# Kernel tuning notes

Hardware: AMD Instinct MI355X
Metric: run time of the kernel (lower is better)

## Reference

```python
import jax, jax.numpy as jnp
import numpy as np

N, T, HW = 32, 46, 128
VOCAB_Q, NUM_ANS = 96, 32
WVEC, RNN_DIM = 32, 128
CNN_DIM, G_DIM, F_DIM = 24, 256, 256
G_IN = 2 * (CNN_DIM + 2) + RNN_DIM  # 180
BN_EPS = 1e-5


def setup_inputs() -> dict:
    key = jax.random.key(0)
    ks = jax.random.split(key, 16)
    s = 0.05
    rn = lambda k, shape: jax.random.normal(k, shape, dtype=jnp.float32) * s
    z = lambda shape: jnp.zeros(shape, jnp.float32)
    o = lambda shape: jnp.ones(shape, jnp.float32)
    inp = {}
    inp['questions'] = jax.random.randint(ks[0], (N, T), 1, VOCAB_Q)  # no NULL padding -> last step is the valid hidden state
    inp['images'] = jax.random.normal(ks[1], (N, 3, HW, HW), dtype=jnp.float32)
    inp['embed_W'] = rn(ks[2], (VOCAB_Q, WVEC))
    inp['lstm_Wih'] = rn(ks[3], (4 * RNN_DIM, WVEC))
    inp['lstm_Whh'] = rn(ks[4], (4 * RNN_DIM, RNN_DIM))
    inp['lstm_bih'] = z((4 * RNN_DIM,))
    inp['lstm_bhh'] = z((4 * RNN_DIM,))
    inp['conv0_W'] = rn(ks[5], (CNN_DIM, 3, 3, 3))
    inp['conv0_b'] = z((CNN_DIM,))
    inp['bn0_g'] = o((CNN_DIM,))
    inp['bn0_b'] = z((CNN_DIM,))
    inp['convs_W'] = rn(ks[6], (3, CNN_DIM, CNN_DIM, 3, 3))
    inp['convs_b'] = z((3, CNN_DIM))
    inp['bns_g'] = o((3, CNN_DIM))
    inp['bns_b'] = z((3, CNN_DIM))
    inp['g0_W'] = rn(ks[7], (G_DIM, G_IN))
    inp['g0_b'] = z((G_DIM,))
    inp['gs_W'] = rn(ks[8], (3, G_DIM, G_DIM))
    inp['gs_b'] = z((3, G_DIM))
    inp['f0_W'] = rn(ks[9], (F_DIM, G_DIM))
    inp['f0_b'] = z((F_DIM,))
    inp['f1_W'] = rn(ks[10], (F_DIM, F_DIM))
    inp['f1_b'] = z((F_DIM,))
    inp['f2_W'] = rn(ks[11], (NUM_ANS, F_DIM))
    inp['f2_b'] = z((NUM_ANS,))
    return inp


def _dense(x, W, b):
    return x @ W.T + b


def _lstm_last(emb, Wih, Whh, bih, bhh):
    # emb: (N, T, D); single-layer LSTM, PyTorch gate order (i, f, g, o); return last hidden state
    n, h = emb.shape[0], Whh.shape[1]
    bias = bih + bhh

    def step(carry, x_t):
        hp, cp = carry
        zg = x_t @ Wih.T + hp @ Whh.T + bias
        i, f, g, o_ = jnp.split(zg, 4, axis=-1)
        c = jax.nn.sigmoid(f) * cp + jax.nn.sigmoid(i) * jnp.tanh(g)
        hn = jax.nn.sigmoid(o_) * jnp.tanh(c)
        return (hn, c), None

    init = (jnp.zeros((n, h), emb.dtype), jnp.zeros((n, h), emb.dtype))
    (h_last, _), _ = jax.lax.scan(step, init, jnp.swapaxes(emb, 0, 1))
    return h_last


def _conv_bn_relu(x, W, b, gamma, beta):
    # Conv2d(k=3, s=2, p=1) + BatchNorm2d (training-mode batch stats) + ReLU
    x = jax.lax.conv_general_dilated(x, W, window_strides=(2, 2), padding=((1, 1), (1, 1)),
                                     dimension_numbers=('NCHW', 'OIHW', 'NCHW'))
    x = x + b[None, :, None, None]
    mu = x.mean((0, 2, 3), keepdims=True)
    var = ((x - mu) ** 2).mean((0, 2, 3), keepdims=True)  # biased var, as torch BN
    x = (x - mu) * jax.lax.rsqrt(var + BN_EPS)
    x = x * gamma[None, :, None, None] + beta[None, :, None, None]
    return jax.nn.relu(x)


def _forward(questions, images, embed_W, lstm_Wih, lstm_Whh, lstm_bih, lstm_bhh,
             conv0_W, conv0_b, bn0_g, bn0_b, convs_W, convs_b, bns_g, bns_b,
             g0_W, g0_b, gs_W, gs_b, f0_W, f0_b, f1_W, f1_b, f2_W, f2_b):
    # question encoder
    q_feats = _lstm_last(embed_W[questions], lstm_Wih, lstm_Whh, lstm_bih, lstm_bhh)  # (N, rnn_dim)
    # CNN stem
    x = _conv_bn_relu(images, conv0_W, conv0_b, bn0_g, bn0_b)
    for i in range(3):
        x = _conv_bn_relu(x, convs_W[i], convs_b[i], bns_g[i], bns_b[i])
    n, c, h, w = x.shape
    m = h * w
    # append normalized coordinates
    xc = jnp.broadcast_to(jnp.linspace(0.0, 1.0, w, dtype=x.dtype).reshape(1, 1, 1, w), (n, 1, h, w))
    yc = jnp.broadcast_to(jnp.linspace(0.0, 1.0, h, dtype=x.dtype).reshape(1, 1, h, 1), (n, 1, h, w))
    objects = jnp.concatenate([x, xc, yc], axis=1).reshape(n, c + 2, m)
    objects = jnp.swapaxes(objects, 1, 2)  # (N, M, C+2)
    # all M^2 ordered pairs: pairs[n, i*M+j] = [obj_i, obj_j]
    feats1 = jnp.repeat(objects, m, axis=1)        # (N, M^2, C+2)
    feats2 = jnp.tile(objects, (1, m, 1))          # (N, M^2, C+2)
    q_rep = jnp.broadcast_to(q_feats[:, None, :], (n, m * m, q_feats.shape[-1]))
    g_in = jnp.concatenate([feats1, feats2, q_rep], axis=-1)  # (N, M^2, 180)
    # shared MLP g
    hidden = jax.nn.relu(_dense(g_in, g0_W, g0_b))
    for i in range(3):
        hidden = jax.nn.relu(_dense(hidden, gs_W[i], gs_b[i]))
    f_in = hidden.sum(axis=1)  # old-torch sum(1) kept dim then [:,0] -> (N, g_dim)
    # MLP f (dropout = identity at eval)
    hidden = jax.nn.relu(_dense(f_in, f0_W, f0_b))
    hidden = jax.nn.relu(_dense(hidden, f1_W, f1_b))
    return _dense(hidden, f2_W, f2_b)  # (N, num_answers)


def reference(questions, images, embed_W, lstm_Wih, lstm_Whh, lstm_bih, lstm_bhh,
              conv0_W, conv0_b, bn0_g, bn0_b, convs_W, convs_b, bns_g, bns_b,
              g0_W, g0_b, gs_W, gs_b, f0_W, f0_b, f1_W, f1_b, f2_W, f2_b):
    return _forward(questions, images, embed_W, lstm_Wih, lstm_Whh, lstm_bih, lstm_bhh,
                    conv0_W, conv0_b, bn0_g, bn0_b, convs_W, convs_b, bns_g, bns_b,
                    g0_W, g0_b, gs_W, gs_b, f0_W, f0_b, f1_W, f1_b, f2_W, f2_b)
```

## Files before the change

### kernel.cpp

```cpp
#include <hip/hip_runtime.h>

#define NB   32
#define TT   46
#define RNN  128
#define CDIM 24
#define GD   256
#define GIN  180

typedef __attribute__((ext_vector_type(8))) short  bf16x8;
typedef __attribute__((ext_vector_type(4))) short  s16x4;
typedef __attribute__((ext_vector_type(8))) unsigned short u16x8;
typedef __attribute__((ext_vector_type(4))) float  f32x4;

__device__ __forceinline__ unsigned short f2bf(float v) {
    unsigned u = __float_as_uint(v);
    u = u + 0x7fffu + ((u >> 16) & 1u);
    return (unsigned short)(u >> 16);
}

__device__ __forceinline__ void lstm_body(
    const int* __restrict__ q, const float* __restrict__ embW,
    const float* __restrict__ Wih, const float* __restrict__ Whh,
    const float* __restrict__ bih, const float* __restrict__ bhh,
    float* __restrict__ qf, int n)
{
    const int tid = threadIdx.x;
    __shared__ __align__(16) float xs[32], hs[RNN];
    __shared__ float zg[512];
    f32x4 wih[8], whh[32];
    {
        const f32x4* wp = (const f32x4*)(Wih + tid * 32);
#pragma unroll
        for (int j = 0; j < 8; j++) wih[j] = wp[j];
        const f32x4* hp = (const f32x4*)(Whh + tid * RNN);
#pragma unroll
        for (int j = 0; j < 32; j++) whh[j] = hp[j];
    }
    const float bias = bih[tid] + bhh[tid];
    float creg = 0.f;
    if (tid < RNN) hs[tid] = 0.f;
    float xr = (tid < 32) ? embW[q[n * TT] * 32 + tid] : 0.f;
    __syncthreads();
    for (int t = 0; t < TT; t++) {
        if (tid < 32) xs[tid] = xr;
        __syncthreads();
        if (tid < 32 && t + 1 < TT) xr = embW[q[n * TT + t + 1] * 32 + tid];
        const f32x4* h4 = (const f32x4*)hs;
        const f32x4* x4 = (const f32x4*)xs;
        f32x4 a0 = {0.f, 0.f, 0.f, 0.f}, a1 = a0, a2 = a0, a3 = a0;
#pragma unroll
        for (int j = 0; j < 8; j += 4) {
            a0 += wih[j] * x4[j];     a1 += wih[j + 1] * x4[j + 1];
            a2 += wih[j + 2] * x4[j + 2]; a3 += wih[j + 3] * x4[j + 3];
        }
#pragma unroll
        for (int j = 0; j < 32; j += 4) {
            a0 += whh[j] * h4[j];     a1 += whh[j + 1] * h4[j + 1];
            a2 += whh[j + 2] * h4[j + 2]; a3 += whh[j + 3] * h4[j + 3];
        }
        f32x4 a = (a0 + a1) + (a2 + a3);
        zg[tid] = bias + ((a[0] + a[1]) + (a[2] + a[3]));
        __syncthreads();
        if (tid < RNN) {
            float ig = 1.f / (1.f + __expf(-zg[tid]));
            float fg = 1.f / (1.f + __expf(-zg[RNN + tid]));
            float gg = tanhf(zg[2 * RNN + tid]);
            float og = 1.f / (1.f + __expf(-zg[3 * RNN + tid]));
            float cn = fg * creg + ig * gg;
            creg = cn;
            hs[tid] = og * tanhf(cn);
        }
        __syncthreads();
    }
    if (tid < RNN) qf[n * RNN + tid] = hs[tid];
}

template<int CIN, int TILE, bool BNIN, int BS>
__device__ __forceinline__ void conv_body(
    const float* __restrict__ in, const float* __restrict__ Wg,
    const float* __restrict__ bias,
    const float* __restrict__ pstats, const float* __restrict__ pg,
    const float* __restrict__ pb, float pinvM,
    float* __restrict__ out, float* __restrict__ stats,
    int HIN, int WIN, int HO, int WO, int tilesX, int bx)
{
    constexpr int NPIX = TILE * TILE;
    constexpr int CPG  = BS / NPIX;
    constexpr int COPT = 24 / CPG;
    constexpr int WPB  = BS / 64;
    constexpr int WPC  = NPIX / 64;
    constexpr int S  = 2 * TILE + 1;
    constexpr int SP = S + 1;
    __shared__ float in_t[CIN][S][SP];
    __shared__ float r1s[WPB][COPT], r2s[WPB][COPT];
    __shared__ float sc[CIN], sh[CIN];
    const int tid = threadIdx.x;
    const int tx = bx % tilesX;
    const int ty = (bx / tilesX) % tilesX;
    const int n  = bx / (tilesX * tilesX);

    if (BNIN) {
        if (tid < CIN) {
            float mu  = pstats[2 * tid] * pinvM;
            float var = pstats[2 * tid + 1] * pinvM - mu * mu;
            float rs  = rsqrtf(var + 1e-5f);
            sc[tid] = rs * pg[tid];
            sh[tid] = pb[tid] - mu * rs * pg[tid];
        }
        __syncthreads();
    }
    const int iy0 = ty * 2 * TILE - 1, ix0 = tx * 2 * TILE - 1;
    for (int idx = tid; idx < CIN * S * S; idx += BS) {
        int ci = idx / (S * S), r = idx % (S * S);
        int ry = r / S, rx = r % S;
        int gy = iy0 + ry, gx = ix0 + rx;
        float v = 0.f;
        if ((unsigned)gy < (unsigned)HIN && (unsigned)gx < (unsigned)WIN) {
            v = in[((size_t)(n * CIN + ci) * HIN + gy) * WIN + gx];
            if (BNIN) v = fmaxf(v * sc[ci] + sh[ci], 0.f);
        }
        in_t[ci][ry][rx] = v;
    }
    __syncthreads();

    const int p   = tid % NPIX;
    const int co0 = __builtin_amdgcn_readfirstlane((tid / NPIX) * COPT);
    const int ly  = (p / TILE) * 2, lx = (p % TILE) * 2;
    float acc[COPT];
#pragma unroll
    for (int c = 0; c < COPT; c++) acc[c] = bias[co0 + c];
    for (int ci = 0; ci < CIN; ci++) {
#pragma unroll
        for (int ky = 0; ky < 3; ky++) {
            const float* row = &in_t[ci][ly + ky][lx];
#pragma unroll
            for (int kx = 0; kx < 3; kx++) {
                float v = row[kx];
#pragma unroll
                for (int c = 0; c < COPT; c++)
                    acc[c] += v * Wg[(((co0 + c) * CIN + ci) * 3 + ky) * 3 + kx];
            }
        }
    }
    const int oy = ty * TILE + p / TILE, ox = tx * TILE + p % TILE;
#pragma unroll
    for (int c = 0; c < COPT; c++)
        out[((size_t)(n * 24 + co0 + c) * HO + oy) * WO + ox] = acc[c];

    const int lane = tid & 63, wv = tid >> 6;
#pragma unroll
    for (int c = 0; c < COPT; c++) {
        float s1 = acc[c], s2 = acc[c] * acc[c];
#pragma unroll
        for (int off = 1; off < 64; off <<= 1) {
            s1 += __shfl_xor(s1, off, 64);
            s2 += __shfl_xor(s2, off, 64);
        }
        if (lane == 0) { r1s[wv][c] = s1; r2s[wv][c] = s2; }
    }
    __syncthreads();
    if (tid < 24) {
        int cg = tid / COPT, slot = tid % COPT;
        float t1 = 0.f, t2 = 0.f;
#pragma unroll
        for (int u = 0; u < WPC; u++) { t1 += r1s[cg * WPC + u][slot]; t2 += r2s[cg * WPC + u][slot]; }
        atomicAdd(&stats[tid * 2],     t1);
        atomicAdd(&stats[tid * 2 + 1], t2);
    }
}

template<int CIN, int TILE, bool BNIN>
__global__ __launch_bounds__(256) void conv_tiled(
    const float* __restrict__ in, const float* __restrict__ Wg,
    const float* __restrict__ bias,
    const float* __restrict__ pstats, const float* __restrict__ pg,
    const float* __restrict__ pb, float pinvM,
    float* __restrict__ out, float* __restrict__ stats,
    int HIN, int WIN, int HO, int WO, int tilesX)
{
    conv_body<CIN, TILE, BNIN, 256>(in, Wg, bias, pstats, pg, pb, pinvM,
                                    out, stats, HIN, WIN, HO, WO, tilesX, blockIdx.x);
}

__global__ __launch_bounds__(512, 2) void fused_front(
    const int* __restrict__ q, const float* __restrict__ embW,
    const float* __restrict__ Wih, const float* __restrict__ Whh,
    const float* __restrict__ bih, const float* __restrict__ bhh,
    float* __restrict__ qf,
    const float* __restrict__ images, const float* __restrict__ c0W,
    const float* __restrict__ c0b, float* __restrict__ conv0o,
    float* __restrict__ stats,
    const float* __restrict__ gsW, unsigned short* __restrict__ Wbf)
{
    const int bx = blockIdx.x;
    if (bx < 32) {
        lstm_body(q, embW, Wih, Whh, bih, bhh, qf, bx);
    } else if (bx < 544) {
        conv_body<3, 16, false, 512>(images, c0W, c0b, nullptr, nullptr, nullptr, 0.f,
                                     conv0o, stats, 128, 128, 64, 64, 4, bx - 32);
    } else {
        int i = ((bx - 544) << 9) + threadIdx.x;
#pragma unroll
        for (int u = 0; u < 4; u++) {
            Wbf[i] = f2bf(gsW[i]);
            i += 96 * 512;
        }
    }
}

__global__ __launch_bounds__(256) void abqt_kernel(
    const float* __restrict__ feat,
    const float* __restrict__ stats, const float* __restrict__ g,
    const float* __restrict__ b, float invM,
    const float* __restrict__ qf,
    const float* __restrict__ g0W,
    const float* __restrict__ g0b,
    float* __restrict__ A, float* __restrict__ Bm, float* __restrict__ QT)
{
    const int n = blockIdx.x >> 2, iq = blockIdx.x & 3, k = threadIdx.x;
    __shared__ float wAB[256][53];
    __shared__ float wq[64][128];
    __shared__ float obj[16][28];
    __shared__ float qs[RNN];
    __shared__ float sc[24], sh[24];
    if (k < 24) {
        float mu  = stats[2 * k] * invM;
        float var = stats[2 * k + 1] * invM - mu * mu;
        float rs  = rsqrtf(var + 1e-5f);
        sc[k] = rs * g[k];
        sh[k] = b[k] - mu * rs * g[k];
    }
    if (k >= 128) qs[k - 128] = qf[n * RNN + (k - 128)];
    for (int idx = k; idx < 256 * 52; idx += 256) {
        int kr = idx / 52, c = idx % 52;
        wAB[kr][c] = g0W[kr * GIN + c];
    }
    for (int idx = k; idx < 64 * 128; idx += 256) {
        int r = idx >> 7, d = idx & 127;
        wq[r][d] = g0W[(((iq << 6) + r)) * GIN + 52 + d];
    }
    __syncthreads();
    for (int idx = k; idx < 24 * 16; idx += 256) {
        int c = idx >> 4, il = idx & 15;
        int i = (iq << 4) + il;
        float v = feat[(n * CDIM + c) * 64 + i];
        obj[il][c] = fmaxf(v * sc[c] + sh[c], 0.f);
    }
    if (k < 16) {
        int i = (iq << 4) + k;
        obj[k][24] = (float)(i & 7)  * (1.f / 7.f);
        obj[k][25] = (float)(i >> 3) * (1.f / 7.f);
        obj[k][26] = 0.f; obj[k][27] = 0.f;
    }
    __syncthreads();
    if (k < 64) {
        int kr = (iq << 6) + k;
        float qv = g0b[kr];
#pragma unroll
        for (int d = 0; d < RNN; d++) qv += wq[k][d] * qs[d];
        QT[(n << 8) + kr] = qv;
    }
    float wA[26], wB[26];
#pragma unroll
    for (int c = 0; c < 26; c++) { wA[c] = wAB[k][c]; wB[c] = wAB[k][26 + c]; }
    for (int il = 0; il < 16; il++) {
        const f32x4* op = (const f32x4*)obj[il];
        f32x4 r0 = op[0], r1 = op[1], r2 = op[2], r3 = op[3],
              r4 = op[4], r5 = op[5], r6 = op[6];
        float a = 0.f, bb = 0.f;
#pragma unroll
        for (int p = 0; p < 4; p++) {
            a += wA[p] * r0[p] + wA[4 + p] * r1[p] + wA[8 + p] * r2[p]
               + wA[12 + p] * r3[p] + wA[16 + p] * r4[p] + wA[20 + p] * r5[p];
            bb += wB[p] * r0[p] + wB[4 + p] * r1[p] + wB[8 + p] * r2[p]
                + wB[12 + p] * r3[p] + wB[16 + p] * r4[p] + wB[20 + p] * r5[p];
        }
        a += wA[24] * r6[0] + wA[25] * r6[1];
        bb += wB[24] * r6[0] + wB[25] * r6[1];
        int i = (iq << 4) + il;
        A [(((n << 6) + i) << 8) + k] = a;
        Bm[(((n << 6) + i) << 8) + k] = bb;
    }
}

__global__ __launch_bounds__(256, 2) void gs_fused(
    const float* __restrict__ A, const float* __restrict__ Bm, const float* __restrict__ QT,
    const unsigned short* __restrict__ Wb,
    const float* __restrict__ gsb,
    float* __restrict__ partial)
{
    __shared__ __align__(16) unsigned short Xs[128 * 256];
    __shared__ float AQ[2][256];
    __shared__ float biasv[3][256];
    const int raw = blockIdx.x;
    const int bb = (raw & 7) * 128 + (raw >> 3);
    const int n = bb >> 5, ip = bb & 31, tid = threadIdx.x;
    const int lane = tid & 63, w = tid >> 6, l15 = lane & 15, lh = lane >> 4;

    {
        float qt = QT[(n << 8) + tid];
        AQ[0][tid] = A[(((n << 6) + ip * 2)     << 8) + tid] + qt;
        AQ[1][tid] = A[(((n << 6) + ip * 2 + 1) << 8) + tid] + qt;
        biasv[0][tid] = gsb[tid];
        biasv[1][tid] = gsb[256 + tid];
        biasv[2][tid] = gsb[512 + tid];
    }
    __syncthreads();

#pragma unroll
    for (int it = 0; it < 16; it++) {
        int task = tid + (it << 8);
        int r = task >> 5, g = task & 31;
        int isub = r >> 6, j = r & 63;
        const f32x4* bp = (const f32x4*)(Bm + (((n << 6) + j) << 8) + (g << 3));
        f32x4 b0 = bp[0], b1 = bp[1];
        u16x8 pk;
        int c0 = g << 3;
#pragma unroll
        for (int p = 0; p < 4; p++) {
            pk[p]     = f2bf(fmaxf(b0[p] + AQ[isub][c0 + p], 0.f));
            pk[p + 4] = f2bf(fmaxf(b1[p] + AQ[isub][c0 + 4 + p], 0.f));
        }
        *(u16x8*)((char*)Xs + r * 512 + ((g ^ (r & 7)) << 4)) = pk;
    }

    f32x4 acc[4][8];
    const f32x4 zero4 = {0.f, 0.f, 0.f, 0.f};
    bf16x8 wa[4], wn[4], xa[8], xn[8];
    for (int layer = 0; layer < 3; layer++) {
#pragma unroll
        for (int tc = 0; tc < 4; tc++)
#pragma unroll
            for (int sl = 0; sl < 8; sl++) acc[tc][sl] = zero4;
        const unsigned short* wbase = Wb + (layer << 16)
                                    + (((w << 6) + l15) << 8) + (lh << 3);
#pragma unroll
        for (int tc = 0; tc < 4; tc++) wa[tc] = *(const bf16x8*)(wbase + (tc << 12));
        __syncthreads();
#pragma unroll
        for (int sl = 0; sl < 8; sl++) {
            int ar = (sl << 4) + l15;
            int au = lh ^ (ar & 7);
            xa[sl] = *(const bf16x8*)((const char*)Xs + ar * 512 + (au << 4));
        }
#pragma unroll
        for (int kb = 0; kb < 8; kb++) {
            if (kb < 7) {
#pragma unroll
                for (int tc = 0; tc < 4; tc++)
                    wn[tc] = *(const bf16x8*)(wbase + (tc << 12) + ((kb + 1) << 5));
#pragma unroll
                for (int sl = 0; sl < 8; sl++) {
                    int ar = (sl << 4) + l15;
                    int au = (((kb + 1) << 2) + lh) ^ (ar & 7);
                    xn[sl] = *(const bf16x8*)((const char*)Xs + ar * 512 + (au << 4));
                }
            }
#pragma unroll
            for (int tc = 0; tc < 4; tc++)
#pragma unroll
                for (int sl = 0; sl < 8; sl++)
                    acc[tc][sl] = __builtin_amdgcn_mfma_f32_16x16x32_bf16(
                        wa[tc], xa[sl], acc[tc][sl], 0, 0, 0);
            if (kb < 7) {
#pragma unroll
                for (int tc = 0; tc < 4; tc++) wa[tc] = wn[tc];
#pragma unroll
                for (int sl = 0; sl < 8; sl++) xa[sl] = xn[sl];
            }
        }
        if (layer < 2) {
            __syncthreads();
#pragma unroll
            for (int tc = 0; tc < 4; tc++) {
                int c0 = (w << 6) + (tc << 4) + (lh << 2);
                float b0 = biasv[layer][c0],     b1 = biasv[layer][c0 + 1];
                float b2 = biasv[layer][c0 + 2], b3 = biasv[layer][c0 + 3];
#pragma unroll
                for (int sl = 0; sl < 8; sl++) {
                    int row = (sl << 4) + l15;
                    s16x4 pk;
                    pk[0] = (short)f2bf(fmaxf(acc[tc][sl][0] + b0, 0.f));
                    pk[1] = (short)f2bf(fmaxf(acc[tc][sl][1] + b1, 0.f));
                    pk[2] = (short)f2bf(fmaxf(acc[tc][sl][2] + b2, 0.f));
                    pk[3] = (short)f2bf(fmaxf(acc[tc][sl][3] + b3, 0.f));
                    *(s16x4*)((char*)Xs + row * 512 + (((c0 >> 3) ^ (row & 7)) << 4)
                              + ((c0 & 7) << 1)) = pk;
                }
            }
        } else {
#pragma unroll
            for (int tc = 0; tc < 4; tc++) {
                int c0 = (w << 6) + (tc << 4) + (lh << 2);
                f32x4 cs;
#pragma unroll
                for (int p = 0; p < 4; p++) {
                    float bv = biasv[2][c0 + p];
                    float s = 0.f;
#pragma unroll
                    for (int sl = 0; sl < 8; sl++) s += fmaxf(acc[tc][sl][p] + bv, 0.f);
                    s += __shfl_xor(s, 1, 64);
                    s += __shfl_xor(s, 2, 64);
                    s += __shfl_xor(s, 4, 64);
                    s += __shfl_xor(s, 8, 64);
                    cs[p] = s;
                }
                if (l15 == 0) *(f32x4*)(partial + (size_t)bb * 256 + c0) = cs;
            }
        }
    }
}

__device__ __forceinline__ float dot256(const float* __restrict__ wr,
                                        const float* __restrict__ x)
{
    const f32x4* w4 = (const f32x4*)wr;
    const f32x4* x4 = (const f32x4*)x;
    f32x4 a0 = {0.f, 0.f, 0.f, 0.f}, a1 = a0, a2 = a0, a3 = a0;
#pragma unroll 8
    for (int c = 0; c < 64; c += 4) {
        f32x4 w0 = w4[c], w1 = w4[c + 1], w2 = w4[c + 2], w3 = w4[c + 3];
        f32x4 x0 = x4[c], x1 = x4[c + 1], x2 = x4[c + 2], x3 = x4[c + 3];
        a0 += w0 * x0; a1 += w1 * x1; a2 += w2 * x2; a3 += w3 * x3;
    }
    f32x4 a = (a0 + a1) + (a2 + a3);
    return (a[0] + a[1]) + (a[2] + a[3]);
}

__global__ __launch_bounds__(256) void f_mlp(
    const float* __restrict__ partial,
    const float* __restrict__ f0W, const float* __restrict__ f0b,
    const float* __restrict__ f1W, const float* __restrict__ f1b,
    const float* __restrict__ f2W, const float* __restrict__ f2b,
    float* __restrict__ out)
{
    const int n = blockIdx.x, k = threadIdx.x;
    __shared__ float fin[256], h1[256], h2[256];
    const float* pb = partial + (size_t)(n * 32) * 256 + k;
    float s0 = 0.f, s1 = 0.f, s2 = 0.f, s3 = 0.f;
#pragma unroll
    for (int b = 0; b < 32; b += 4) {
        s0 += pb[(b + 0) << 8];
        s1 += pb[(b + 1) << 8];
        s2 += pb[(b + 2) << 8];
        s3 += pb[(b + 3) << 8];
    }
    fin[k] = (s0 + s1) + (s2 + s3);
    __syncthreads();
    h1[k] = fmaxf(dot256(f0W + (k << 8), fin) + f0b[k], 0.f);
    __syncthreads();
    h2[k] = fmaxf(dot256(f1W + (k << 8), h1) + f1b[k], 0.f);
    __syncthreads();
    if (k < 32)
        out[(n << 5) + k] = dot256(f2W + (k << 8), h2) + f2b[k];
}

extern "C" void kernel_launch(void* const* d_in, const int* in_sizes, int n_in,
                              void* d_out, int out_size, void* d_ws, size_t ws_size,
                              hipStream_t stream)
{
    const int*   questions = (const int*)  d_in[0];
    const float* images = (const float*)d_in[1];
    const float* embW   = (const float*)d_in[2];
    const float* Wih    = (const float*)d_in[3];
    const float* Whh    = (const float*)d_in[4];
    const float* bih    = (const float*)d_in[5];
    const float* bhh    = (const float*)d_in[6];
    const float* c0W    = (const float*)d_in[7];
    const float* c0b    = (const float*)d_in[8];
    const float* bn0g   = (const float*)d_in[9];
    const float* bn0b   = (const float*)d_in[10];
    const float* csW    = (const float*)d_in[11];
    const float* csb    = (const float*)d_in[12];
    const float* bnsg   = (const float*)d_in[13];
    const float* bnsb   = (const float*)d_in[14];
    const float* g0W    = (const float*)d_in[15];
    const float* g0b    = (const float*)d_in[16];
    const float* gsW    = (const float*)d_in[17];
    const float* gsb    = (const float*)d_in[18];
    const float* f0W    = (const float*)d_in[19];
    const float* f0b    = (const float*)d_in[20];
    const float* f1W    = (const float*)d_in[21];
    const float* f1b    = (const float*)d_in[22];
    const float* f2W    = (const float*)d_in[23];
    const float* f2b    = (const float*)d_in[24];

    float* ws  = (float*)d_ws;
    float* out = (float*)d_out;

    float* conv0o = ws;
    float* conv1o = ws + 3145728;
    float* conv2o = ws + 3932160;
    float* conv3o = ws + 4128768;
    float* stats  = ws + 4177920;
    float* qf     = ws + 4178112;
    unsigned short* Wbf = (unsigned short*)(ws + 4182208);
    float* Abuf   = ws;
    float* Bbuf   = ws + 524288;
    float* QTb    = ws + 1048576;
    float* part   = ws + 1155072;

    hipMemsetAsync(stats, 0, 192 * sizeof(float), stream);

    fused_front<<<640, 512, 0, stream>>>(questions, embW, Wih, Whh, bih, bhh, qf,
                                         images, c0W, c0b, conv0o, stats, gsW, Wbf);
    conv_tiled<24, 8, true><<<512, 256, 0, stream>>>(
        conv0o, csW, csb, stats, bn0g, bn0b, 1.f / 131072.f,
        conv1o, stats + 48, 64, 64, 32, 32, 4);
    conv_tiled<24, 8, true><<<128, 256, 0, stream>>>(
        conv1o, csW + 5184, csb + 24, stats + 48, bnsg, bnsb, 1.f / 32768.f,
        conv2o, stats + 96, 32, 32, 16, 16, 2);
    conv_tiled<24, 8, true><<<32, 256, 0, stream>>>(
        conv2o, csW + 10368, csb + 48, stats + 96, bnsg + 24, bnsb + 24, 1.f / 8192.f,
        conv3o, stats + 144, 16, 16, 8, 8, 1);

    abqt_kernel<<<128, 256, 0, stream>>>(conv3o, stats + 144, bnsg + 48, bnsb + 48,
                                         1.f / 2048.f, qf, g0W, g0b, Abuf, Bbuf, QTb);
    gs_fused<<<1024, 256, 0, stream>>>(Abuf, Bbuf, QTb, Wbf, gsb, part);
    f_mlp<<<32, 256, 0, stream>>>(part, f0W, f0b, f1W, f1b, f2W, f2b, out);
}
```

Before: 276.7 us.

## Split LSTM gate dot products across thread pairs and re-tile gs_fused MFMA

The LSTM now gives each gate row to two threads, each holding half the weights, and combines them with a shuffle. This halves register pressure and lets fused_front run 1024-thread blocks, with the conv0 and weight-conversion block counts adjusted to match. In gs_fused, each wave now owns 32 rows across all 256 output columns instead of 64 columns across all 128 rows. Weights are loaded straight from global memory per k-block with no prefetch, and the final column sums are reduced across waves through a small shared buffer.

```diff
diff --git a/kernel.cpp b/kernel.cpp
--- a/kernel.cpp
+++ b/kernel.cpp
@@ -25,18 +25,19 @@
     float* __restrict__ qf, int n)
 {
     const int tid = threadIdx.x;
+    const int g = tid >> 1, h = tid & 1;
     __shared__ __align__(16) float xs[32], hs[RNN];
     __shared__ float zg[512];
-    f32x4 wih[8], whh[32];
+    f32x4 wih[4], whh[16];
     {
-        const f32x4* wp = (const f32x4*)(Wih + tid * 32);
-#pragma unroll
-        for (int j = 0; j < 8; j++) wih[j] = wp[j];
-        const f32x4* hp = (const f32x4*)(Whh + tid * RNN);
-#pragma unroll
-        for (int j = 0; j < 32; j++) whh[j] = hp[j];
-    }
-    const float bias = bih[tid] + bhh[tid];
+        const f32x4* wp = (const f32x4*)(Wih + g * 32 + h * 16);
+#pragma unroll
+        for (int j = 0; j < 4; j++) wih[j] = wp[j];
+        const f32x4* hp = (const f32x4*)(Whh + g * RNN + h * 64);
+#pragma unroll
+        for (int j = 0; j < 16; j++) whh[j] = hp[j];
+    }
+    const float bias = bih[g] + bhh[g];
     float creg = 0.f;
     if (tid < RNN) hs[tid] = 0.f;
     float xr = (tid < 32) ? embW[q[n * TT] * 32 + tid] : 0.f;
@@ -45,21 +46,20 @@
         if (tid < 32) xs[tid] = xr;
         __syncthreads();
         if (tid < 32 && t + 1 < TT) xr = embW[q[n * TT + t + 1] * 32 + tid];
-        const f32x4* h4 = (const f32x4*)hs;
-        const f32x4* x4 = (const f32x4*)xs;
+        const f32x4* x4 = (const f32x4*)xs + (h << 2);
+        const f32x4* h4 = (const f32x4*)hs + (h << 4);
         f32x4 a0 = {0.f, 0.f, 0.f, 0.f}, a1 = a0, a2 = a0, a3 = a0;
-#pragma unroll
-        for (int j = 0; j < 8; j += 4) {
-            a0 += wih[j] * x4[j];     a1 += wih[j + 1] * x4[j + 1];
-            a2 += wih[j + 2] * x4[j + 2]; a3 += wih[j + 3] * x4[j + 3];
-        }
-#pragma unroll
-        for (int j = 0; j < 32; j += 4) {
-            a0 += whh[j] * h4[j];     a1 += whh[j + 1] * h4[j + 1];
+        a0 += wih[0] * x4[0]; a1 += wih[1] * x4[1];
+        a2 += wih[2] * x4[2]; a3 += wih[3] * x4[3];
+#pragma unroll
+        for (int j = 0; j < 16; j += 4) {
+            a0 += whh[j] * h4[j];         a1 += whh[j + 1] * h4[j + 1];
             a2 += whh[j + 2] * h4[j + 2]; a3 += whh[j + 3] * h4[j + 3];
         }
         f32x4 a = (a0 + a1) + (a2 + a3);
-        zg[tid] = bias + ((a[0] + a[1]) + (a[2] + a[3]));
+        float p = (a[0] + a[1]) + (a[2] + a[3]);
+        p += __shfl_xor(p, 1, 64);
+        if (h == 0) zg[g] = p + bias;
         __syncthreads();
         if (tid < RNN) {
             float ig = 1.f / (1.f + __expf(-zg[tid]));
@@ -182,7 +182,7 @@
                                     out, stats, HIN, WIN, HO, WO, tilesX, blockIdx.x);
 }
 
-__global__ __launch_bounds__(512, 2) void fused_front(
+__global__ __launch_bounds__(1024, 4) void fused_front(
     const int* __restrict__ q, const float* __restrict__ embW,
     const float* __restrict__ Wih, const float* __restrict__ Whh,
     const float* __restrict__ bih, const float* __restrict__ bhh,
@@ -196,14 +196,14 @@
     if (bx < 32) {
         lstm_body(q, embW, Wih, Whh, bih, bhh, qf, bx);
     } else if (bx < 544) {
-        conv_body<3, 16, false, 512>(images, c0W, c0b, nullptr, nullptr, nullptr, 0.f,
-                                     conv0o, stats, 128, 128, 64, 64, 4, bx - 32);
+        conv_body<3, 16, false, 1024>(images, c0W, c0b, nullptr, nullptr, nullptr, 0.f,
+                                      conv0o, stats, 128, 128, 64, 64, 4, bx - 32);
     } else {
-        int i = ((bx - 544) << 9) + threadIdx.x;
+        int i = ((bx - 544) << 10) + threadIdx.x;
 #pragma unroll
         for (int u = 0; u < 4; u++) {
             Wbf[i] = f2bf(gsW[i]);
-            i += 96 * 512;
+            i += 48 * 1024;
         }
     }
 }
@@ -292,6 +292,7 @@
     __shared__ __align__(16) unsigned short Xs[128 * 256];
     __shared__ float AQ[2][256];
     __shared__ float biasv[3][256];
+    __shared__ float red[4][256];
     const int raw = blockIdx.x;
     const int bb = (raw & 7) * 128 + (raw >> 3);
     const int n = bb >> 5, ip = bb & 31, tid = threadIdx.x;
@@ -324,89 +325,82 @@
         *(u16x8*)((char*)Xs + r * 512 + ((g ^ (r & 7)) << 4)) = pk;
     }
 
-    f32x4 acc[4][8];
+    f32x4 acc[16][2];
     const f32x4 zero4 = {0.f, 0.f, 0.f, 0.f};
-    bf16x8 wa[4], wn[4], xa[8], xn[8];
     for (int layer = 0; layer < 3; layer++) {
 #pragma unroll
-        for (int tc = 0; tc < 4; tc++)
-#pragma unroll
-            for (int sl = 0; sl < 8; sl++) acc[tc][sl] = zero4;
-        const unsigned short* wbase = Wb + (layer << 16)
-                                    + (((w << 6) + l15) << 8) + (lh << 3);
-#pragma unroll
-        for (int tc = 0; tc < 4; tc++) wa[tc] = *(const bf16x8*)(wbase + (tc << 12));
+        for (int tc = 0; tc < 16; tc++) { acc[tc][0] = zero4; acc[tc][1] = zero4; }
+        const unsigned short* wbase = Wb + (layer << 16) + (l15 << 8) + (lh << 3);
         __syncthreads();
-#pragma unroll
-        for (int sl = 0; sl < 8; sl++) {
-            int ar = (sl << 4) + l15;
+        bf16x8 xa[2], xn[2];
+#pragma unroll
+        for (int sl = 0; sl < 2; sl++) {
+            int ar = (w << 5) + (sl << 4) + l15;
             int au = lh ^ (ar & 7);
             xa[sl] = *(const bf16x8*)((const char*)Xs + ar * 512 + (au << 4));
         }
 #pragma unroll
         for (int kb = 0; kb < 8; kb++) {
+            bf16x8 wa[16];
+#pragma unroll
+            for (int tc = 0; tc < 16; tc++)
+                wa[tc] = *(const bf16x8*)(wbase + (tc << 12) + (kb << 5));
             if (kb < 7) {
 #pragma unroll
-                for (int tc = 0; tc < 4; tc++)
-                    wn[tc] = *(const bf16x8*)(wbase + (tc << 12) + ((kb + 1) << 5));
-#pragma unroll
-                for (int sl = 0; sl < 8; sl++) {
-                    int ar = (sl << 4) + l15;
+                for (int sl = 0; sl < 2; sl++) {
+                    int ar = (w << 5) + (sl << 4) + l15;
                     int au = (((kb + 1) << 2) + lh) ^ (ar & 7);
                     xn[sl] = *(const bf16x8*)((const char*)Xs + ar * 512 + (au << 4));
                 }
             }
 #pragma unroll
-            for (int tc = 0; tc < 4; tc++)
-#pragma unroll
-                for (int sl = 0; sl < 8; sl++)
-                    acc[tc][sl] = __builtin_amdgcn_mfma_f32_16x16x32_bf16(
-                        wa[tc], xa[sl], acc[tc][sl], 0, 0, 0);
-            if (kb < 7) {
-#pragma unroll
-                for (int tc = 0; tc < 4; tc++) wa[tc] = wn[tc];
-#pragma unroll
-                for (int sl = 0; sl < 8; sl++) xa[sl] = xn[sl];
+            for (int tc = 0; tc < 16; tc++) {
+                acc[tc][0] = __builtin_amdgcn_mfma_f32_16x16x32_bf16(
+                    wa[tc], xa[0], acc[tc][0], 0, 0, 0);
+                acc[tc][1] = __builtin_amdgcn_mfma_f32_16x16x32_bf16(
+                    wa[tc], xa[1], acc[tc][1], 0, 0, 0);
             }
+            if (kb < 7) { xa[0] = xn[0]; xa[1] = xn[1]; }
         }
         if (layer < 2) {
             __syncthreads();
 #pragma unroll
-            for (int tc = 0; tc < 4; tc++) {
-                int c0 = (w << 6) + (tc << 4) + (lh << 2);
-                float b0 = biasv[layer][c0],     b1 = biasv[layer][c0 + 1];
-                float b2 = biasv[layer][c0 + 2], b3 = biasv[layer][c0 + 3];
-#pragma unroll
-                for (int sl = 0; sl < 8; sl++) {
-                    int row = (sl << 4) + l15;
+            for (int tc = 0; tc < 16; tc++) {
+                int c0 = (tc << 4) + (lh << 2);
+                f32x4 bv = *(const f32x4*)&biasv[layer][c0];
+#pragma unroll
+                for (int sl = 0; sl < 2; sl++) {
+                    int row = (w << 5) + (sl << 4) + l15;
                     s16x4 pk;
-                    pk[0] = (short)f2bf(fmaxf(acc[tc][sl][0] + b0, 0.f));
-                    pk[1] = (short)f2bf(fmaxf(acc[tc][sl][1] + b1, 0.f));
-                    pk[2] = (short)f2bf(fmaxf(acc[tc][sl][2] + b2, 0.f));
-                    pk[3] = (short)f2bf(fmaxf(acc[tc][sl][3] + b3, 0.f));
+                    pk[0] = (short)f2bf(fmaxf(acc[tc][sl][0] + bv[0], 0.f));
+                    pk[1] = (short)f2bf(fmaxf(acc[tc][sl][1] + bv[1], 0.f));
+                    pk[2] = (short)f2bf(fmaxf(acc[tc][sl][2] + bv[2], 0.f));
+                    pk[3] = (short)f2bf(fmaxf(acc[tc][sl][3] + bv[3], 0.f));
                     *(s16x4*)((char*)Xs + row * 512 + (((c0 >> 3) ^ (row & 7)) << 4)
                               + ((c0 & 7) << 1)) = pk;
                 }
             }
         } else {
 #pragma unroll
-            for (int tc = 0; tc < 4; tc++) {
-                int c0 = (w << 6) + (tc << 4) + (lh << 2);
-                f32x4 cs;
+            for (int tc = 0; tc < 16; tc++) {
+                int c0 = (tc << 4) + (lh << 2);
+                f32x4 bv = *(const f32x4*)&biasv[2][c0];
+                f32x4 v;
 #pragma unroll
                 for (int p = 0; p < 4; p++) {
-                    float bv = biasv[2][c0 + p];
-                    float s = 0.f;
-#pragma unroll
-                    for (int sl = 0; sl < 8; sl++) s += fmaxf(acc[tc][sl][p] + bv, 0.f);
+                    float s = fmaxf(acc[tc][0][p] + bv[p], 0.f)
+                            + fmaxf(acc[tc][1][p] + bv[p], 0.f);
                     s += __shfl_xor(s, 1, 64);
                     s += __shfl_xor(s, 2, 64);
                     s += __shfl_xor(s, 4, 64);
                     s += __shfl_xor(s, 8, 64);
-                    cs[p] = s;
+                    v[p] = s;
                 }
-                if (l15 == 0) *(f32x4*)(partial + (size_t)bb * 256 + c0) = cs;
+                if (l15 == 0) *(f32x4*)&red[w][c0] = v;
             }
+            __syncthreads();
+            partial[(size_t)bb * 256 + tid] =
+                red[0][tid] + red[1][tid] + red[2][tid] + red[3][tid];
         }
     }
 }
@@ -502,8 +496,8 @@
 
     hipMemsetAsync(stats, 0, 192 * sizeof(float), stream);
 
-    fused_front<<<640, 512, 0, stream>>>(questions, embW, Wih, Whh, bih, bhh, qf,
-                                         images, c0W, c0b, conv0o, stats, gsW, Wbf);
+    fused_front<<<592, 1024, 0, stream>>>(questions, embW, Wih, Whh, bih, bhh, qf,
+                                          images, c0W, c0b, conv0o, stats, gsW, Wbf);
     conv_tiled<24, 8, true><<<512, 256, 0, stream>>>(
         conv0o, csW, csb, stats, bn0g, bn0b, 1.f / 131072.f,
         conv1o, stats + 48, 64, 64, 32, 32, 4);
```

Result: slower. 446.9 us (+61.5%).

## Use fast LSTM activations, relax front occupancy, keep A+Q in registers

Applied to the files above, without the earlier changes.

The LSTM gate activations now use exp-based sigmoid and tanh in place of tanhf, which shortens the serial recurrence. The fused front kernel's launch bound drops from 2 to 1 blocks per SM, giving the compiler more registers. In gs_fused, each thread loads its own A+QT slice into registers, so the AQ shared buffer and one block barrier go away. The exp-based tanh may lose a little accuracy, and lower occupancy can hurt the conv part of the front kernel.

```diff
diff --git a/kernel.cpp b/kernel.cpp
--- a/kernel.cpp
+++ b/kernel.cpp
@@ -16,6 +16,13 @@
     unsigned u = __float_as_uint(v);
     u = u + 0x7fffu + ((u >> 16) & 1u);
     return (unsigned short)(u >> 16);
+}
+
+__device__ __forceinline__ float fast_sigmoid(float x) {
+    return 1.f / (1.f + __expf(-x));
+}
+__device__ __forceinline__ float fast_tanh(float x) {
+    return 1.f - 2.f / (__expf(2.f * x) + 1.f);
 }
 
 __device__ __forceinline__ void lstm_body(
@@ -62,13 +69,13 @@
         zg[tid] = bias + ((a[0] + a[1]) + (a[2] + a[3]));
         __syncthreads();
         if (tid < RNN) {
-            float ig = 1.f / (1.f + __expf(-zg[tid]));
-            float fg = 1.f / (1.f + __expf(-zg[RNN + tid]));
-            float gg = tanhf(zg[2 * RNN + tid]);
-            float og = 1.f / (1.f + __expf(-zg[3 * RNN + tid]));
+            float ig = fast_sigmoid(zg[tid]);
+            float fg = fast_sigmoid(zg[RNN + tid]);
+            float gg = fast_tanh(zg[2 * RNN + tid]);
+            float og = fast_sigmoid(zg[3 * RNN + tid]);
             float cn = fg * creg + ig * gg;
             creg = cn;
-            hs[tid] = og * tanhf(cn);
+            hs[tid] = og * fast_tanh(cn);
         }
         __syncthreads();
     }
@@ -182,7 +189,7 @@
                                     out, stats, HIN, WIN, HO, WO, tilesX, blockIdx.x);
 }
 
-__global__ __launch_bounds__(512, 2) void fused_front(
+__global__ __launch_bounds__(512, 1) void fused_front(
     const int* __restrict__ q, const float* __restrict__ embW,
     const float* __restrict__ Wih, const float* __restrict__ Whh,
     const float* __restrict__ bih, const float* __restrict__ bhh,
@@ -290,38 +297,40 @@
     float* __restrict__ partial)
 {
     __shared__ __align__(16) unsigned short Xs[128 * 256];
-    __shared__ float AQ[2][256];
     __shared__ float biasv[3][256];
     const int raw = blockIdx.x;
     const int bb = (raw & 7) * 128 + (raw >> 3);
     const int n = bb >> 5, ip = bb & 31, tid = threadIdx.x;
     const int lane = tid & 63, w = tid >> 6, l15 = lane & 15, lh = lane >> 4;
 
+    biasv[0][tid] = gsb[tid];
+    biasv[1][tid] = gsb[256 + tid];
+    biasv[2][tid] = gsb[512 + tid];
+
     {
-        float qt = QT[(n << 8) + tid];
-        AQ[0][tid] = A[(((n << 6) + ip * 2)     << 8) + tid] + qt;
-        AQ[1][tid] = A[(((n << 6) + ip * 2 + 1) << 8) + tid] + qt;
-        biasv[0][tid] = gsb[tid];
-        biasv[1][tid] = gsb[256 + tid];
-        biasv[2][tid] = gsb[512 + tid];
-    }
-    __syncthreads();
-
-#pragma unroll
-    for (int it = 0; it < 16; it++) {
-        int task = tid + (it << 8);
-        int r = task >> 5, g = task & 31;
-        int isub = r >> 6, j = r & 63;
-        const f32x4* bp = (const f32x4*)(Bm + (((n << 6) + j) << 8) + (g << 3));
-        f32x4 b0 = bp[0], b1 = bp[1];
-        u16x8 pk;
-        int c0 = g << 3;
-#pragma unroll
-        for (int p = 0; p < 4; p++) {
-            pk[p]     = f2bf(fmaxf(b0[p] + AQ[isub][c0 + p], 0.f));
-            pk[p + 4] = f2bf(fmaxf(b1[p] + AQ[isub][c0 + 4 + p], 0.f));
-        }
-        *(u16x8*)((char*)Xs + r * 512 + ((g ^ (r & 7)) << 4)) = pk;
+        const int g = tid & 31, c0 = g << 3;
+        const f32x4* qtp = (const f32x4*)(QT + (n << 8) + c0);
+        f32x4 qta = qtp[0], qtb = qtp[1];
+        const f32x4* a0p = (const f32x4*)(A + (((n << 6) + ip * 2)     << 8) + c0);
+        const f32x4* a1p = (const f32x4*)(A + (((n << 6) + ip * 2 + 1) << 8) + c0);
+        f32x4 aq0a = a0p[0] + qta, aq0b = a0p[1] + qtb;
+        f32x4 aq1a = a1p[0] + qta, aq1b = a1p[1] + qtb;
+#pragma unroll
+        for (int it = 0; it < 16; it++) {
+            int r = (tid >> 5) + (it << 3);
+            int j = r & 63;
+            f32x4 aa = (it < 8) ? aq0a : aq1a;
+            f32x4 ab = (it < 8) ? aq0b : aq1b;
+            const f32x4* bp = (const f32x4*)(Bm + (((n << 6) + j) << 8) + c0);
+            f32x4 b0 = bp[0], b1 = bp[1];
+            u16x8 pk;
+#pragma unroll
+            for (int p = 0; p < 4; p++) {
+                pk[p]     = f2bf(fmaxf(b0[p] + aa[p], 0.f));
+                pk[p + 4] = f2bf(fmaxf(b1[p] + ab[p], 0.f));
+            }
+            *(u16x8*)((char*)Xs + r * 512 + ((g ^ (r & 7)) << 4)) = pk;
+        }
     }
 
     f32x4 acc[4][8];
```

Measured after the change: 274.0 us, median of 4. No clear change (-1.0%).
